# Kernel tuning notes

Hardware: AMD Instinct MI355X
Metric: run time of the kernel (lower is better)

Reference implementation:

```python
import jax, jax.numpy as jnp
import numpy as np

N = 50000      # nodes
E = 800000     # edges
MUL = 32       # multiplicity of each irrep (32x0e + 32x1o)
SQRT3 = 3.0 ** 0.5


def setup_inputs() -> dict:
    key = jax.random.key(0)
    k = jax.random.split(key, 7)
    node_features = jax.random.normal(k[0], (N, 4 * MUL), dtype=jnp.float32)  # [N, 32 + 32*3]
    positions = jax.random.normal(k[1], (N, 3), dtype=jnp.float32)
    edge_src = jax.random.randint(k[2], (E,), 0, N, dtype=jnp.int32)
    edge_dst = jax.random.randint(k[3], (E,), 0, N, dtype=jnp.int32)
    tp_weight = jax.random.normal(k[4], (4 * MUL,), dtype=jnp.float32)  # tp.weight_numel = 128
    W_s = jax.random.normal(k[5], (2 * MUL, MUL), dtype=jnp.float32)    # linear: mid 0e (2 blocks) -> out 0e
    W_v = jax.random.normal(k[6], (2 * MUL, MUL), dtype=jnp.float32)    # linear: mid 1o (2 blocks) -> out 1o
    return dict(node_features=node_features, positions=positions,
                edge_src=edge_src, edge_dst=edge_dst,
                tp_weight=tp_weight, W_s=W_s, W_v=W_v)


def reference(node_features, positions, edge_src, edge_dst, tp_weight, W_s, W_v):
    # --- edge vectors and spherical harmonics (normalize=True, 'component') ---
    edge_vec = positions[edge_dst] - positions[edge_src]                       # [E,3]
    unit = edge_vec * jax.lax.rsqrt(jnp.sum(edge_vec * edge_vec, -1, keepdims=True) + 1e-12)
    sh1 = SQRT3 * unit                                                         # l=1 SH, component norm; sh0 == 1
    # --- gather source node features, split irreps ---
    src = node_features[edge_src]                                              # [E,128]
    s = src[:, :MUL]                                                           # [E,32]  scalars 32x0e
    v = src[:, MUL:].reshape(-1, MUL, 3)                                       # [E,32,3] vectors 32x1o
    w0, w1, w2, w3 = jnp.split(tp_weight, 4)                                   # per-path 'uvu' weights (u=32, v=1)
    # --- CG tensor product paths ---
    mid0 = w0 * s                                                              # 0e x 0e -> 0e
    mid1 = (w1 * s)[:, :, None] * sh1[:, None, :]                              # 0e x 1o -> 1o
    mid2 = w2[None, :, None] * v                                               # 1o x 0e -> 1o
    mid3 = w3 * (jnp.einsum('eum,em->eu', v, sh1) / SQRT3)                     # 1o x 1o -> 0e (w3j = delta/sqrt(3))
    messages = jnp.concatenate(
        [mid0, mid1.reshape(-1, 3 * MUL), mid2.reshape(-1, 3 * MUL), mid3], axis=-1)  # [E,256]
    # --- scatter-add messages to destination nodes ---
    agg = jax.ops.segment_sum(messages, edge_dst, num_segments=N)              # [N,256]
    a0 = agg[:, :MUL]
    a1 = agg[:, MUL:4 * MUL].reshape(N, MUL, 3)
    a2 = agg[:, 4 * MUL:7 * MUL].reshape(N, MUL, 3)
    a3 = agg[:, 7 * MUL:]
    # --- equivariant linear mix mid -> out (fan-in normalized per irrep) ---
    inv = np.float32(1.0 / np.sqrt(2 * MUL))
    out_s = (jnp.concatenate([a0, a3], axis=-1) @ W_s) * inv                   # [N,32]
    out_v = jnp.einsum('num,uo->nom', jnp.concatenate([a1, a2], axis=1), W_v) * inv  # [N,32,3]
    return jnp.concatenate([out_s, out_v.reshape(N, 3 * MUL)], axis=-1)        # [N,128]
```

## Files before the change

### kernel.cpp

```cpp
#include <hip/hip_runtime.h>
#include <hip/hip_fp16.h>

#define SQRT3 1.7320508075688772f
#define INV_SQRT3 0.5773502691896258f
#define CAP 64

#define WAVE_SYNC() do { asm volatile("s_waitcnt lgkmcnt(0)" ::: "memory"); \
                         __builtin_amdgcn_wave_barrier(); } while (0)

__global__ void prep_kernel(const float* __restrict__ feat, const float* __restrict__ pos,
                            const float* __restrict__ Ws, const float* __restrict__ Wv,
                            const float* __restrict__ tpw,
                            uint2* __restrict__ featH, float4* __restrict__ pos4,
                            int* __restrict__ cnt,
                            float* __restrict__ WS, float* __restrict__ WV, int N) {
    int i = blockIdx.x * blockDim.x + threadIdx.x;
    int totalF = N * 32;
    if (i < totalF) {
        int node = i >> 5, cl = i & 31;
        const float* fb = feat + (size_t)node * 128;
        float s  = fb[cl];
        float v0 = fb[32 + 3 * cl], v1 = fb[33 + 3 * cl], v2 = fb[34 + 3 * cl];
        __half2 h0 = __floats2half2_rn(s, v0);
        __half2 h1 = __floats2half2_rn(v1, v2);
        uint2 r;
        r.x = *(const unsigned int*)&h0;
        r.y = *(const unsigned int*)&h1;
        featH[i] = r;
        return;
    }
    int j = i - totalF;
    if (j < 32) {
        featH[totalF + j] = make_uint2(0u, 0u);
        return;
    }
    j -= 32;
    if (j < N) {
        pos4[j] = make_float4(pos[3 * j], pos[3 * j + 1], pos[3 * j + 2], 0.f);
        cnt[j] = 0;
        return;
    }
    int k = j - N;
    if (k < 2048) {
        int u = k >> 5;
        float ws = Ws[k], wv = Wv[k];
        if (u < 32) {
            WS[k] = 0.125f * tpw[u] * ws;
            WV[k] = 0.125f * tpw[32 + u] * wv;
        } else {
            int uu = u - 32;
            WS[k] = 0.125f * tpw[96 + uu] * INV_SQRT3 * ws;
            WV[k] = 0.125f * tpw[64 + uu] * wv;
        }
    }
}

__global__ void scatter_kernel(const int* __restrict__ esrc, const int* __restrict__ edst,
                               int* __restrict__ cnt, int* __restrict__ csrP, int E) {
    int t = blockIdx.x * blockDim.x + threadIdx.x;
    int e0 = t * 4;
    if (e0 + 4 <= E) {
        int4 s4 = *(const int4*)(esrc + e0);
        int4 d4 = *(const int4*)(edst + e0);
        int p;
        p = atomicAdd(&cnt[d4.x], 1); if (p < CAP) csrP[(size_t)d4.x * CAP + p] = s4.x;
        p = atomicAdd(&cnt[d4.y], 1); if (p < CAP) csrP[(size_t)d4.y * CAP + p] = s4.y;
        p = atomicAdd(&cnt[d4.z], 1); if (p < CAP) csrP[(size_t)d4.z * CAP + p] = s4.z;
        p = atomicAdd(&cnt[d4.w], 1); if (p < CAP) csrP[(size_t)d4.w * CAP + p] = s4.w;
    } else {
        for (int e = e0; e < E; ++e) {
            int d = edst[e];
            int p = atomicAdd(&cnt[d], 1);
            if (p < CAP) csrP[(size_t)d * CAP + p] = esrc[e];
        }
    }
}


__global__ __launch_bounds__(256) void node_kernel(
    const uint2* __restrict__ featH, const float4* __restrict__ pos4,
    const int* __restrict__ csrP, const int* __restrict__ cnt,
    const float* __restrict__ WS, const float* __restrict__ WV,
    float* __restrict__ out, int N)
{
    __shared__ float4 geom[4][64];
    __shared__ float  sS[4][68], sX[4][68], sY[4][68], sZ[4][68];
    int lane = threadIdx.x & 63;
    int w    = threadIdx.x >> 6;
    int node = blockIdx.x * 4 + w;
    if (node >= N) return;

    int deg = cnt[node];
    int len = deg < CAP ? deg : CAP;
    int lenP = (len + 7) & ~7;
    int half = lane >> 5;
    int cl   = lane & 31;

    float4 pd = pos4[node];

    if (lane < len) {
        int s = csrP[(size_t)node * CAP + lane];
        float4 ps = pos4[s];
        float ex = pd.x - ps.x, ey = pd.y - ps.y, ez = pd.z - ps.z;
        float rr = SQRT3 * rsqrtf(ex * ex + ey * ey + ez * ez + 1e-12f);
        geom[w][lane] = make_float4(rr * ex, rr * ey, rr * ez, __int_as_float(s));
    } else {
        geom[w][lane] = make_float4(0.f, 0.f, 0.f, __int_as_float(N));
    }
    WAVE_SYNC();

    float A0 = 0.f, A1x = 0.f, A1y = 0.f, A1z = 0.f;
    float V0 = 0.f, V1 = 0.f, V2 = 0.f, T3 = 0.f;

    #pragma unroll 4
    for (int m = 0; m + 2 <= lenP; m += 2) {
        float4 g = geom[w][m + half];
        int si = __float_as_int(g.w);
        uint2 fr = featH[(size_t)si * 32 + cl];
        float2 lo = __half22float2(*(const __half2*)&fr.x);
        float2 hi = __half22float2(*(const __half2*)&fr.y);
        A0 += lo.x;
        A1x = fmaf(lo.x, g.x, A1x); A1y = fmaf(lo.x, g.y, A1y); A1z = fmaf(lo.x, g.z, A1z);
        V0 += lo.y; V1 += hi.x; V2 += hi.y;
        T3 = fmaf(lo.y, g.x, fmaf(hi.x, g.y, fmaf(hi.y, g.z, T3)));
    }

    A0 += __shfl_xor(A0, 32);  A1x += __shfl_xor(A1x, 32);
    A1y += __shfl_xor(A1y, 32); A1z += __shfl_xor(A1z, 32);
    V0 += __shfl_xor(V0, 32);  V1 += __shfl_xor(V1, 32);
    V2 += __shfl_xor(V2, 32);  T3 += __shfl_xor(T3, 32);

    int k = half ? (32 + cl) : cl;
    sS[w][k] = half ? T3 : A0;
    sX[w][k] = half ? V0 : A1x;
    sY[w][k] = half ? V1 : A1y;
    sZ[w][k] = half ? V2 : A1z;
    WAVE_SYNC();

    size_t ob = (size_t)node * 128;
    #pragma unroll
    for (int t = 0; t < 2; ++t) {
        int j = lane + 64 * t;
        const float *ap, *wp;
        if (j < 32) {
            ap = sS[w]; wp = WS + j;
        } else {
            int v = j - 32;
            int o = v / 3, mm = v - 3 * o;
            ap = (mm == 0) ? sX[w] : (mm == 1) ? sY[w] : sZ[w];
            wp = WV + o;
        }
        float r = 0.f;
        #pragma unroll
        for (int q = 0; q < 16; ++q) {
            float4 a = *(const float4*)(ap + 4 * q);
            r = fmaf(a.x, wp[(4 * q + 0) * 32], r);
            r = fmaf(a.y, wp[(4 * q + 1) * 32], r);
            r = fmaf(a.z, wp[(4 * q + 2) * 32], r);
            r = fmaf(a.w, wp[(4 * q + 3) * 32], r);
        }
        out[ob + j] = r;
    }
}

extern "C" void kernel_launch(void* const* d_in, const int* in_sizes, int n_in,
                              void* d_out, int out_size, void* d_ws, size_t ws_size,
                              hipStream_t stream) {
    const float* feat = (const float*)d_in[0];
    const float* pos  = (const float*)d_in[1];
    const int*   esrc = (const int*)d_in[2];
    const int*   edst = (const int*)d_in[3];
    const float* tpw  = (const float*)d_in[4];
    const float* Ws   = (const float*)d_in[5];
    const float* Wv   = (const float*)d_in[6];
    float* out = (float*)d_out;

    int N = in_sizes[0] / 128;
    int E = in_sizes[2];

    uint2*  featH = (uint2*)d_ws;
    float4* pos4  = (float4*)(featH + (size_t)(N + 1) * 32);
    int*    csrP  = (int*)(pos4 + N);
    int*    cnt   = csrP + (size_t)N * CAP;
    float*  WS    = (float*)(cnt + N);
    float*  WV    = WS + 2048;

    const int tb = 256;
    int prepTot = N * 32 + 32 + N + 2048;
    int ebk = (E / 4 + tb) / tb;
    prep_kernel<<<(prepTot + tb - 1) / tb, tb, 0, stream>>>(feat, pos, Ws, Wv, tpw,
                                                            featH, pos4, cnt, WS, WV, N);
    scatter_kernel<<<ebk, tb, 0, stream>>>(esrc, edst, cnt, csrP, E);
    node_kernel<<<(N + 3) / 4, 256, 0, stream>>>(featH, pos4, csrP, cnt, WS, WV, out, N);
}
```

Measured before the change: 133.6 us.

## Compute edge geometry during scatter and store packed half-precision slots

The edge unit-vector computation moves from the node kernel into the scatter kernel. Each bucket slot now holds the half-precision direction together with a 16-bit source index, so the node kernel reads geometry straight from global memory and no longer runs the per-edge position gather, the LDS staging and the wave sync. The scatter pass now does two random position gathers per edge and writes 8-byte slots instead of 4-byte ones. The path is used only when N fits in 16 bits and the workspace is large enough, and it adds half-precision rounding to the edge directions.

```diff
diff --git a/kernel.cpp b/kernel.cpp
--- a/kernel.cpp
+++ b/kernel.cpp
@@ -30,10 +30,7 @@
         return;
     }
     int j = i - totalF;
-    if (j < 32) {
-        featH[totalF + j] = make_uint2(0u, 0u);
-        return;
-    }
+    if (j < 32) { featH[totalF + j] = make_uint2(0u, 0u); return; }
     j -= 32;
     if (j < N) {
         pos4[j] = make_float4(pos[3 * j], pos[3 * j + 1], pos[3 * j + 2], 0.f);
@@ -52,6 +49,34 @@
             WS[k] = 0.125f * tpw[96 + uu] * INV_SQRT3 * ws;
             WV[k] = 0.125f * tpw[64 + uu] * wv;
         }
+    }
+}
+
+__global__ void scatter_gg_kernel(const int* __restrict__ esrc, const int* __restrict__ edst,
+                                  const float4* __restrict__ pos4,
+                                  int* __restrict__ cnt, uint2* __restrict__ geomH, int E) {
+    int t = blockIdx.x * blockDim.x + threadIdx.x;
+    int e0 = t * 4;
+    auto doEdge = [&](int s, int d) {
+        int p = atomicAdd(&cnt[d], 1);
+        if (p < CAP) {
+            float4 pd = pos4[d], ps = pos4[s];
+            float ex = pd.x - ps.x, ey = pd.y - ps.y, ez = pd.z - ps.z;
+            float rr = SQRT3 * rsqrtf(ex * ex + ey * ey + ez * ez + 1e-12f);
+            __half2 hxy = __floats2half2_rn(rr * ex, rr * ey);
+            __half  hz  = __float2half_rn(rr * ez);
+            uint2 g;
+            g.x = *(const unsigned int*)&hxy;
+            g.y = (unsigned)(*(const unsigned short*)&hz) | ((unsigned)s << 16);
+            geomH[(size_t)d * CAP + p] = g;
+        }
+    };
+    if (e0 + 4 <= E) {
+        int4 s4 = *(const int4*)(esrc + e0);
+        int4 d4 = *(const int4*)(edst + e0);
+        doEdge(s4.x, d4.x); doEdge(s4.y, d4.y); doEdge(s4.z, d4.z); doEdge(s4.w, d4.w);
+    } else {
+        for (int e = e0; e < E; ++e) doEdge(esrc[e], edst[e]);
     }
 }
 
@@ -77,13 +102,15 @@
 }
 
 
+template<bool GG>
 __global__ __launch_bounds__(256) void node_kernel(
     const uint2* __restrict__ featH, const float4* __restrict__ pos4,
-    const int* __restrict__ csrP, const int* __restrict__ cnt,
+    const int* __restrict__ csrP, const uint2* __restrict__ geomH,
+    const int* __restrict__ cnt,
     const float* __restrict__ WS, const float* __restrict__ WV,
     float* __restrict__ out, int N)
 {
-    __shared__ float4 geom[4][64];
+    __shared__ float4 geom[4][GG ? 1 : 64];
     __shared__ float  sS[4][68], sX[4][68], sY[4][68], sZ[4][68];
     int lane = threadIdx.x & 63;
     int w    = threadIdx.x >> 6;
@@ -96,33 +123,54 @@
     int half = lane >> 5;
     int cl   = lane & 31;
 
-    float4 pd = pos4[node];
-
-    if (lane < len) {
-        int s = csrP[(size_t)node * CAP + lane];
-        float4 ps = pos4[s];
-        float ex = pd.x - ps.x, ey = pd.y - ps.y, ez = pd.z - ps.z;
-        float rr = SQRT3 * rsqrtf(ex * ex + ey * ey + ez * ez + 1e-12f);
-        geom[w][lane] = make_float4(rr * ex, rr * ey, rr * ez, __int_as_float(s));
-    } else {
-        geom[w][lane] = make_float4(0.f, 0.f, 0.f, __int_as_float(N));
-    }
-    WAVE_SYNC();
-
     float A0 = 0.f, A1x = 0.f, A1y = 0.f, A1z = 0.f;
     float V0 = 0.f, V1 = 0.f, V2 = 0.f, T3 = 0.f;
 
-    #pragma unroll 4
-    for (int m = 0; m + 2 <= lenP; m += 2) {
-        float4 g = geom[w][m + half];
-        int si = __float_as_int(g.w);
-        uint2 fr = featH[(size_t)si * 32 + cl];
-        float2 lo = __half22float2(*(const __half2*)&fr.x);
-        float2 hi = __half22float2(*(const __half2*)&fr.y);
-        A0 += lo.x;
-        A1x = fmaf(lo.x, g.x, A1x); A1y = fmaf(lo.x, g.y, A1y); A1z = fmaf(lo.x, g.z, A1z);
-        V0 += lo.y; V1 += hi.x; V2 += hi.y;
-        T3 = fmaf(lo.y, g.x, fmaf(hi.x, g.y, fmaf(hi.y, g.z, T3)));
+    if constexpr (GG) {
+        const uint2* grow = geomH + (size_t)node * CAP;
+        #pragma unroll 4
+        for (int m = 0; m + 2 <= lenP; m += 2) {
+            int e = m + half;
+            uint2 ge = grow[e];
+            bool ok = e < len;
+            float2 gxy = __half22float2(*(const __half2*)&ge.x);
+            unsigned short uz = (unsigned short)(ge.y & 0xFFFFu);
+            float gz = __half2float(*(const __half*)&uz);
+            int si = ok ? (int)(ge.y >> 16) : 0;
+            unsigned msk = ok ? 0xFFFFFFFFu : 0u;
+            uint2 fr = featH[(size_t)si * 32 + cl];
+            fr.x &= msk; fr.y &= msk;
+            float2 lo = __half22float2(*(const __half2*)&fr.x);
+            float2 hi = __half22float2(*(const __half2*)&fr.y);
+            A0 += lo.x;
+            A1x = fmaf(lo.x, gxy.x, A1x); A1y = fmaf(lo.x, gxy.y, A1y); A1z = fmaf(lo.x, gz, A1z);
+            V0 += lo.y; V1 += hi.x; V2 += hi.y;
+            T3 = fmaf(lo.y, gxy.x, fmaf(hi.x, gxy.y, fmaf(hi.y, gz, T3)));
+        }
+    } else {
+        float4 pd = pos4[node];
+        if (lane < len) {
+            int s = csrP[(size_t)node * CAP + lane];
+            float4 ps = pos4[s];
+            float ex = pd.x - ps.x, ey = pd.y - ps.y, ez = pd.z - ps.z;
+            float rr = SQRT3 * rsqrtf(ex * ex + ey * ey + ez * ez + 1e-12f);
+            geom[w][lane] = make_float4(rr * ex, rr * ey, rr * ez, __int_as_float(s));
+        } else {
+            geom[w][lane] = make_float4(0.f, 0.f, 0.f, __int_as_float(N));
+        }
+        WAVE_SYNC();
+        #pragma unroll 4
+        for (int m = 0; m + 2 <= lenP; m += 2) {
+            float4 g = geom[w][m + half];
+            int si = __float_as_int(g.w);
+            uint2 fr = featH[(size_t)si * 32 + cl];
+            float2 lo = __half22float2(*(const __half2*)&fr.x);
+            float2 hi = __half22float2(*(const __half2*)&fr.y);
+            A0 += lo.x;
+            A1x = fmaf(lo.x, g.x, A1x); A1y = fmaf(lo.x, g.y, A1y); A1z = fmaf(lo.x, g.z, A1z);
+            V0 += lo.y; V1 += hi.x; V2 += hi.y;
+            T3 = fmaf(lo.y, g.x, fmaf(hi.x, g.y, fmaf(hi.y, g.z, T3)));
+        }
     }
 
     A0 += __shfl_xor(A0, 32);  A1x += __shfl_xor(A1x, 32);
@@ -180,16 +228,38 @@
 
     uint2*  featH = (uint2*)d_ws;
     float4* pos4  = (float4*)(featH + (size_t)(N + 1) * 32);
-    int*    csrP  = (int*)(pos4 + N);
-    int*    cnt   = csrP + (size_t)N * CAP;
-    float*  WS    = (float*)(cnt + N);
-    float*  WV    = WS + 2048;
+    char*   rest  = (char*)(pos4 + N);
+
+    size_t slotsGG = (size_t)N * CAP * 8;
+    size_t slotsPL = (size_t)N * CAP * 4;
+    size_t fixed   = (size_t)(N + 1) * 256 + (size_t)N * 16 + (size_t)N * 4 + 16384 + 256;
+    bool gg = (N <= 65535) && (ws_size >= fixed + slotsGG);
+
+    uint2* geomH = nullptr; int* csrP = nullptr; int* cnt; float* WS; float* WV;
+    if (gg) {
+        geomH = (uint2*)rest;
+        cnt   = (int*)(geomH + (size_t)N * CAP);
+    } else {
+        csrP  = (int*)rest;
+        cnt   = csrP + (size_t)N * CAP;
+    }
+    WS = (float*)(cnt + N);
+    WV = WS + 2048;
 
     const int tb = 256;
     int prepTot = N * 32 + 32 + N + 2048;
     int ebk = (E / 4 + tb) / tb;
+    int nblocks = (N + 3) / 4;
+
     prep_kernel<<<(prepTot + tb - 1) / tb, tb, 0, stream>>>(feat, pos, Ws, Wv, tpw,
                                                             featH, pos4, cnt, WS, WV, N);
-    scatter_kernel<<<ebk, tb, 0, stream>>>(esrc, edst, cnt, csrP, E);
-    node_kernel<<<(N + 3) / 4, 256, 0, stream>>>(featH, pos4, csrP, cnt, WS, WV, out, N);
-}
+    if (gg) {
+        scatter_gg_kernel<<<ebk, tb, 0, stream>>>(esrc, edst, pos4, cnt, geomH, E);
+        node_kernel<true><<<nblocks, 256, 0, stream>>>(featH, pos4, csrP, geomH, cnt,
+                                                       WS, WV, out, N);
+    } else {
+        scatter_kernel<<<ebk, tb, 0, stream>>>(esrc, edst, cnt, csrP, E);
+        node_kernel<false><<<nblocks, 256, 0, stream>>>(featH, pos4, csrP, geomH, cnt,
+                                                        WS, WV, out, N);
+    }
+}
```

Measured after the change: 136.3 us. 2.1% more time.
